# Kernel optimization log

Measured on AMD Instinct MI355X. Metric: run time of the kernel, lower is better.

Reference implementation:

```python
import jax, jax.numpy as jnp
import numpy as np

IN_MODES = (40, 32, 25)    # prod = 32000 = num_embeddings
OUT_MODES = (8, 8, 16)     # prod = 1024  = embedding_dim
RANKS = (1, 16, 16, 1)
B, T = 4, 4096


def setup_inputs() -> dict:
    key = jax.random.key(0)
    k0, k1, k2, kid = jax.random.split(key, 4)
    # cores G_k: (r_k, out_k, in_k, r_{k+1}); xavier-ish scale
    def core(k, rk, om, im, rk1):
        fan = rk + om * im * rk1
        scale = jnp.sqrt(6.0 / fan)
        return jax.random.uniform(k, (rk, om, im, rk1), jnp.float32, -scale, scale)
    core0 = core(k0, RANKS[0], OUT_MODES[0], IN_MODES[0], RANKS[1])
    core1 = core(k1, RANKS[1], OUT_MODES[1], IN_MODES[1], RANKS[2])
    core2 = core(k2, RANKS[2], OUT_MODES[2], IN_MODES[2], RANKS[3])
    input_ids = jax.random.randint(kid, (B, T), 0, int(np.prod(IN_MODES)), dtype=jnp.int64)
    return {"core0": core0, "core1": core1, "core2": core2, "input_ids": input_ids}


def reference(core0, core1, core2, input_ids):
    V = int(np.prod(IN_MODES))
    E = int(np.prod(OUT_MODES))
    # TT reconstruction: contract over ranks a,b,c,d (a=d=1),
    # out modes x,y,z first, then in modes p,q,r (matches torch eq order)
    T_full = jnp.einsum('axpb,byqc,czrd->xyzpqr', core0, core1, core2)
    W = T_full.reshape(E, V).T  # (num_embeddings, embedding_dim)
    return W[input_ids]  # (B, T, E)
```

## Files before the change

kernel.cpp:

```cpp
#include <hip/hip_runtime.h>
#include <hip/hip_bf16.h>


#define T12_FLOATS (40 * 32 * 16 * 64)
#define C2T_FLOATS (25 * 16 * 16)

__global__ __launch_bounds__(256) void tt_precompute_kernel(
    const float* __restrict__ core0, const float* __restrict__ core1,
    const float* __restrict__ core2, float* __restrict__ T12,
    float* __restrict__ C2T) {
  if (blockIdx.x == 1280) {
    for (int i = threadIdx.x; i < C2T_FLOATS; i += 256) {
      int r = i >> 8;
      int cz = i & 255;
      C2T[i] = core2[cz * 25 + r];
    }
    return;
  }
  int pq = blockIdx.x;
  int p = pq >> 5;
  int q = pq & 31;

  __shared__ float sA[8 * 16];
  __shared__ float sB[16 * 8 * 16];

  for (int i = threadIdx.x; i < 128; i += 256) {
    int x = i >> 4, b = i & 15;
    sA[i] = core0[(x * 40 + p) * 16 + b];
  }
  for (int i = threadIdx.x; i < 2048; i += 256) {
    int b = i >> 7;
    int yc = i & 127;
    int y = yc >> 4, c = yc & 15;
    sB[i] = core1[((b * 8 + y) * 32 + q) * 16 + c];
  }
  __syncthreads();

  float* dst = T12 + pq * 1024;
  int xy = threadIdx.x & 63;
  int x = xy >> 3, y = xy & 7;
  for (int c = threadIdx.x >> 6; c < 16; c += 4) {
    float acc = 0.f;
#pragma unroll
    for (int b = 0; b < 16; b++) acc += sA[x * 16 + b] * sB[b * 128 + y * 16 + c];
    dst[c * 64 + xy] = acc;
  }
}

__global__ __launch_bounds__(256) void tt_gather_kernel(
    const float* __restrict__ T12, const float* __restrict__ C2T,
    const int* __restrict__ ids, float* __restrict__ out) {
  int wave = threadIdx.x >> 6;
  int lane = threadIdx.x & 63;
  int t = blockIdx.x * 4 + wave;

  int id = ids[t];
  int p = id / 800;
  int rem = id - p * 800;
  int q = rem / 25;
  int r = rem - q * 25;

  const float4* E = (const float4*)(T12 + (p * 32 + q) * 1024);
  const float4* C = (const float4*)(C2T + r * 256);

  int xyg = lane >> 2;
  int zg = lane & 3;

  float acc[4][4];
#pragma unroll
  for (int i = 0; i < 4; i++)
#pragma unroll
    for (int j = 0; j < 4; j++) acc[i][j] = 0.f;

#pragma unroll
  for (int c = 0; c < 16; c++) {
    float4 e4 = E[c * 16 + xyg];
    float4 w4 = C[c * 4 + zg];
    float ev[4] = {e4.x, e4.y, e4.z, e4.w};
    float wv[4] = {w4.x, w4.y, w4.z, w4.w};
#pragma unroll
    for (int i = 0; i < 4; i++)
#pragma unroll
      for (int j = 0; j < 4; j++) acc[i][j] += ev[i] * wv[j];
  }

  float* dst = out + (size_t)t * 1024 + xyg * 64 + zg * 4;
#pragma unroll
  for (int i = 0; i < 4; i++) {
    float4 v = make_float4(acc[i][0], acc[i][1], acc[i][2], acc[i][3]);
    *((float4*)(dst + i * 16)) = v;
  }
}

extern "C" void kernel_launch(void* const* d_in, const int* in_sizes, int n_in,
                              void* d_out, int out_size, void* d_ws, size_t ws_size,
                              hipStream_t stream) {
  const float* core0 = (const float*)d_in[0];
  const float* core1 = (const float*)d_in[1];
  const float* core2 = (const float*)d_in[2];
  const int* ids = (const int*)d_in[3];
  float* out = (float*)d_out;

  float* T12 = (float*)d_ws;
  float* C2T = T12 + T12_FLOATS;

  tt_precompute_kernel<<<dim3(1281), dim3(256), 0, stream>>>(core0, core1, core2, T12, C2T);
  tt_gather_kernel<<<dim3(16384 / 4), dim3(256), 0, stream>>>(T12, C2T, ids, out);
}
```

Measured before the change: 102.7 us.

## Permute T12 layout for coalesced output stores, add prefetch and nontemporal writes

The precompute kernel now writes T12 with a permuted xy index. Each gather lane can then own a contiguous float4 slot, so every store instruction in a wave covers one contiguous 1 KB span instead of strided 64-byte pieces. Output stores use nontemporal builtins to avoid polluting the cache with the large write-once output. The inner contraction is software-pipelined in groups of four, loading the next group's operands before computing on the current one. An occupancy hint is added to the launch bounds. Together these raise register pressure in exchange for better store coalescing and load latency hiding.

New measurement: 102.4 us. No clear change (-0.4%).

```diff
diff --git a/kernel.cpp b/kernel.cpp
--- a/kernel.cpp
+++ b/kernel.cpp
@@ -1,6 +1,7 @@
 #include <hip/hip_runtime.h>
-#include <hip/hip_bf16.h>
 
+
+typedef float vfloat4 __attribute__((ext_vector_type(4)));
 
 #define T12_FLOATS (40 * 32 * 16 * 64)
 #define C2T_FLOATS (25 * 16 * 16)
@@ -39,15 +40,16 @@
   float* dst = T12 + pq * 1024;
   int xy = threadIdx.x & 63;
   int x = xy >> 3, y = xy & 7;
+  int dof = (xy & 15) * 4 + (xy >> 4);
   for (int c = threadIdx.x >> 6; c < 16; c += 4) {
     float acc = 0.f;
 #pragma unroll
     for (int b = 0; b < 16; b++) acc += sA[x * 16 + b] * sB[b * 128 + y * 16 + c];
-    dst[c * 64 + xy] = acc;
+    dst[c * 64 + dof] = acc;
   }
 }
 
-__global__ __launch_bounds__(256) void tt_gather_kernel(
+__global__ __launch_bounds__(256, 4) void tt_gather_kernel(
     const float* __restrict__ T12, const float* __restrict__ C2T,
     const int* __restrict__ ids, float* __restrict__ out) {
   int wave = threadIdx.x >> 6;
@@ -72,23 +74,46 @@
 #pragma unroll
     for (int j = 0; j < 4; j++) acc[i][j] = 0.f;
 
+  float4 e[4], w[4];
 #pragma unroll
-  for (int c = 0; c < 16; c++) {
-    float4 e4 = E[c * 16 + xyg];
-    float4 w4 = C[c * 4 + zg];
-    float ev[4] = {e4.x, e4.y, e4.z, e4.w};
-    float wv[4] = {w4.x, w4.y, w4.z, w4.w};
-#pragma unroll
-    for (int i = 0; i < 4; i++)
-#pragma unroll
-      for (int j = 0; j < 4; j++) acc[i][j] += ev[i] * wv[j];
+  for (int k = 0; k < 4; k++) {
+    e[k] = E[k * 16 + xyg];
+    w[k] = C[k * 4 + zg];
   }
 
-  float* dst = out + (size_t)t * 1024 + xyg * 64 + zg * 4;
+#pragma unroll
+  for (int cc = 0; cc < 4; cc++) {
+    float4 en[4], wn[4];
+    if (cc < 3) {
+#pragma unroll
+      for (int k = 0; k < 4; k++) {
+        en[k] = E[((cc + 1) * 4 + k) * 16 + xyg];
+        wn[k] = C[((cc + 1) * 4 + k) * 4 + zg];
+      }
+    }
+#pragma unroll
+    for (int k = 0; k < 4; k++) {
+      float ev[4] = {e[k].x, e[k].y, e[k].z, e[k].w};
+      float wv[4] = {w[k].x, w[k].y, w[k].z, w[k].w};
+#pragma unroll
+      for (int i = 0; i < 4; i++)
+#pragma unroll
+        for (int j = 0; j < 4; j++) acc[i][j] += ev[i] * wv[j];
+    }
+    if (cc < 3) {
+#pragma unroll
+      for (int k = 0; k < 4; k++) {
+        e[k] = en[k];
+        w[k] = wn[k];
+      }
+    }
+  }
+
+  float* dst = out + (size_t)t * 1024 + lane * 4;
 #pragma unroll
   for (int i = 0; i < 4; i++) {
-    float4 v = make_float4(acc[i][0], acc[i][1], acc[i][2], acc[i][3]);
-    *((float4*)(dst + i * 16)) = v;
+    vfloat4 v = {acc[i][0], acc[i][1], acc[i][2], acc[i][3]};
+    __builtin_nontemporal_store(v, (vfloat4*)(dst + i * 256));
   }
 }
 
```
